# Optimization experiments

Measured on AMD Instinct MI355X. Metric: run time of the kernel, lower is better.

The kernel has to match this reference:

```python
import jax, jax.numpy as jnp
import numpy as np
import math

MAX_P = 150
D_MODEL = 128
N_HEADS = 4
D_HEAD = D_MODEL // N_HEADS
D_MLP = 512
D_MEM = 64
VOCAB = MAX_P + 2  # 152
EQ_TOKEN = MAX_P + 1  # 151
B = 65536


def setup_inputs() -> dict:
    key = jax.random.key(0)
    ks = jax.random.split(key, 20)
    s = 1.0 / math.sqrt(D_MODEL)
    inp = {
        "p_val": jax.random.randint(ks[0], (B,), 0, MAX_P),
        "a": jax.random.randint(ks[1], (B,), 0, MAX_P),
        "b": jax.random.randint(ks[2], (B,), 0, MAX_P),
        # embeddings
        "token_embed": jax.random.normal(ks[3], (VOCAB, D_MODEL), jnp.float32),
        "pos_embed": jax.random.normal(ks[4], (5, D_MODEL), jnp.float32),
        # TitansMemory
        "W_mem": jax.random.normal(ks[5], (D_MODEL, D_MEM), jnp.float32) * s,
        "b_mem": jnp.zeros((D_MEM,), jnp.float32),
        "W_sur": jax.random.normal(ks[6], (D_MEM, D_MODEL), jnp.float32) * (1.0 / math.sqrt(D_MEM)),
        "b_sur": jnp.zeros((D_MODEL,), jnp.float32),
        "W_m2r": jax.random.normal(ks[7], (D_MEM, D_MODEL), jnp.float32) * (1.0 / math.sqrt(D_MEM)),
        "b_m2r": jnp.zeros((D_MODEL,), jnp.float32),
        # attention
        "W_Q": jax.random.normal(ks[8], (N_HEADS, D_MODEL, D_HEAD), jnp.float32) * s,
        "W_K": jax.random.normal(ks[9], (N_HEADS, D_MODEL, D_HEAD), jnp.float32) * s,
        "W_V": jax.random.normal(ks[10], (N_HEADS, D_MODEL, D_HEAD), jnp.float32) * s,
        "W_O": jax.random.normal(ks[11], (N_HEADS, D_HEAD, D_MODEL), jnp.float32) * s,
        # MLP
        "W_mlp1": jax.random.normal(ks[12], (D_MODEL, D_MLP), jnp.float32) * s,
        "b_mlp1": jnp.zeros((D_MLP,), jnp.float32),
        "W_mlp2": jax.random.normal(ks[13], (D_MLP, D_MODEL), jnp.float32) * (1.0 / math.sqrt(D_MLP)),
        "b_mlp2": jnp.zeros((D_MODEL,), jnp.float32),
        # unembed
        "W_un": jax.random.normal(ks[14], (D_MODEL, MAX_P), jnp.float32) * s,
        "b_un": jnp.zeros((MAX_P,), jnp.float32),
    }
    return inp


def reference(p_val, a, b, token_embed, pos_embed, W_mem, b_mem, W_sur, b_sur,
              W_m2r, b_m2r, W_Q, W_K, W_V, W_O, W_mlp1, b_mlp1, W_mlp2, b_mlp2,
              W_un, b_un):
    eq = jnp.full_like(a, EQ_TOKEN)
    tokens = jnp.stack([p_val, a, b, eq], axis=1)            # [B, 4]
    x = token_embed[tokens] + pos_embed[:4][None, :, :]       # [B, 4, D]

    # Titans memory (test-time update) on the modulus token embedding
    x0 = x[:, 0, :]                                           # [B, D]
    z = jax.nn.silu(x0 @ W_mem + b_mem)                       # [B, d_mem]
    pred_x = z @ W_sur + b_sur                                # [B, D]
    update = jax.nn.silu((x0 - pred_x) @ W_mem)               # [B, d_mem]
    mem = (z + update) @ W_m2r + b_m2r                        # [B, D]
    x = x + mem[:, None, :]

    # attention
    q = jnp.einsum('bsd,hdk->bhsk', x, W_Q)
    k = jnp.einsum('bsd,hdk->bhsk', x, W_K)
    v = jnp.einsum('bsd,hdk->bhsk', x, W_V)
    scores = jnp.einsum('bhsk,bhtk->bhst', q, k) / math.sqrt(D_HEAD)
    pattern = jax.nn.softmax(scores, axis=-1)                 # [B, H, 4, 4]
    attn = jnp.einsum('bhst,bhtk->bhsk', pattern, v)
    attn = jnp.einsum('bhsk,hkm->bsm', attn, W_O)             # [B, 4, D]
    x = x + attn

    # MLP
    x = x + jax.nn.relu(x @ W_mlp1 + b_mlp1) @ W_mlp2 + b_mlp2

    # unembed the '=' position
    logits = x[:, 3, :] @ W_un + b_un                         # [B, max_p]
    return logits
```

## Files before the change

kernel.cpp:

```cpp
#include <hip/hip_runtime.h>

#define D      128
#define DM     64
#define DMLP   512
#define PMAX   150
#define VOC    152
#define EQT    151
#define NBATCH 65536

typedef __attribute__((ext_vector_type(8))) __bf16 bf16x8;
typedef __attribute__((ext_vector_type(4))) float  f32x4;

__device__ __forceinline__ float silu_f(float x){ return x / (1.0f + expf(-x)); }

__device__ __forceinline__ void gl_lds16(const void* g, void* l) {
    __builtin_amdgcn_global_load_lds(
        (const __attribute__((address_space(1))) void*)g,
        (__attribute__((address_space(3))) void*)l, 16, 0, 0);
}

#define OFF_MEMVEC 0
#define OFF_X3BASE 19200
#define OFF_KE     19328
#define OFF_KP     38784
#define OFF_SC     39296
#define OFF_O0     132896
#define OFF_O1     171296
#define OFF_O2     209696
#define OFF_O3     248096
#define OFF_M3B    248352
#define OFF_W1F    257952
#define OFF_W2F    290720
#define OFF_WUF    323488

__global__ void k_P1a(const float* __restrict__ tok, const float* __restrict__ pos,
                      const float* __restrict__ W_mem, const float* __restrict__ b_mem,
                      const float* __restrict__ W_sur, const float* __restrict__ b_sur,
                      const float* __restrict__ W_m2r, const float* __restrict__ b_m2r,
                      const float* __restrict__ W_K,
                      float* __restrict__ memvec, float* __restrict__ x3base,
                      float* __restrict__ KE, float* __restrict__ KP)
{
    int r = blockIdx.x, t = threadIdx.x;
    if (r < 150) {
        int p = r;
        __shared__ float sx0[D], sz[DM], sdiff[D], szu[DM], red4[4][DM], red2[2][D];
        if (t < D) sx0[t] = tok[p*D + t] + pos[t];
        __syncthreads();
        {
            int out = t & 63, seg = t >> 6, k0 = seg*32;
            float acc = 0.f;
            for (int k = 0; k < 32; k++) acc += sx0[k0+k] * W_mem[(k0+k)*DM + out];
            red4[seg][out] = acc;
        }
        __syncthreads();
        if (t < DM) sz[t] = silu_f(b_mem[t] + red4[0][t] + red4[1][t] + red4[2][t] + red4[3][t]);
        __syncthreads();
        {
            int out = t & 127, seg = t >> 7, j0 = seg*32;
            float acc = 0.f;
            for (int j = 0; j < 32; j++) acc += sz[j0+j] * W_sur[(j0+j)*D + out];
            red2[seg][out] = acc;
        }
        __syncthreads();
        if (t < D) sdiff[t] = sx0[t] - (b_sur[t] + red2[0][t] + red2[1][t]);
        __syncthreads();
        {
            int out = t & 63, seg = t >> 6, k0 = seg*32;
            float acc = 0.f;
            for (int k = 0; k < 32; k++) acc += sdiff[k0+k] * W_mem[(k0+k)*DM + out];
            red4[seg][out] = acc;
        }
        __syncthreads();
        if (t < DM) szu[t] = sz[t] + silu_f(red4[0][t] + red4[1][t] + red4[2][t] + red4[3][t]);
        __syncthreads();
        {
            int out = t & 127, seg = t >> 7, j0 = seg*32;
            float acc = 0.f;
            for (int j = 0; j < 32; j++) acc += szu[j0+j] * W_m2r[(j0+j)*D + out];
            red2[seg][out] = acc;
        }
        __syncthreads();
        if (t < D) memvec[p*D + t] = b_m2r[t] + red2[0][t] + red2[1][t];
    } else if (r == 150) {
        if (t < D) x3base[t] = tok[EQT*D + t] + pos[3*D + t];
    } else {
        int idx = r - 151;
        const float* src = (idx < 152) ? (tok + idx*D) : (pos + (idx-152)*D);
        float*       dst = (idx < 152) ? (KE + idx*D)  : (KP + (idx-152)*D);
        __shared__ float s[D], red2[2][D];
        if (t < D) s[t] = src[t];
        __syncthreads();
        {
            int out = t & 127, seg = t >> 7, h = out >> 5, kk = out & 31, d0 = seg*64;
            float acc = 0.f;
            for (int d = 0; d < 64; d++) acc += s[d0+d] * W_K[h*4096 + (d0+d)*32 + kk];
            red2[seg][out] = acc;
        }
        __syncthreads();
        if (t < D) dst[t] = red2[0][t] + red2[1][t];
    }
}

__global__ void k_P2x(const float* __restrict__ memvec, const float* __restrict__ x3base,
                      const float* __restrict__ W_Q, const float* __restrict__ W_V,
                      const float* __restrict__ W_O,
                      const float* __restrict__ KE, const float* __restrict__ KP,
                      const float* __restrict__ tok, const float* __restrict__ pos,
                      const float* __restrict__ W1, const float* __restrict__ W2,
                      const float* __restrict__ WU,
                      float* __restrict__ SC, __bf16* __restrict__ M3B,
                      __bf16* __restrict__ O0, __bf16* __restrict__ O1,
                      __bf16* __restrict__ O2, __bf16* __restrict__ O3,
                      __bf16* __restrict__ W1f, __bf16* __restrict__ W2f, __bf16* __restrict__ WUf)
{
    int r = blockIdx.x, t = threadIdx.x;
    if (r < 300) {
        int p = r >> 1, half = r & 1;
        __shared__ float sMem[D], sIn[D], sQ3[D], sMV[D], redM[2][D];
        if (t < D) { float m = memvec[p*D + t]; sMem[t] = m; sIn[t] = m + x3base[t]; }
        __syncthreads();
        if (t < D) {
            int h = t >> 5, k = t & 31;
            float acc = 0.f;
            for (int d = 0; d < D; d++) acc += sIn[d] * W_Q[h*4096 + d*32 + k];
            sQ3[t] = acc;
        } else {
            int c = t - D; int h = c >> 5, k = c & 31;
            float acc = 0.f;
            for (int d = 0; d < D; d++) acc += sMem[d] * W_V[h*4096 + d*32 + k];
            sMV[c] = acc;
        }
        __syncthreads();
        const float scale = 0.17677669529663687f;
        for (int ii = t; ii < 312; ii += 256) {
            int i = half*312 + ii;
            int v = i >> 2, h = i & 3;
            const float4* qh = (const float4*)(sQ3 + h*32);
            float4 s4 = {0.f, 0.f, 0.f, 0.f};
            if (v < 152) {
                const float4* ke = (const float4*)(KE + v*D + h*32);
                #pragma unroll
                for (int k = 0; k < 8; k++) {
                    float4 q = qh[k], e = ke[k];
                    s4.x += q.x*e.x; s4.y += q.y*e.y; s4.z += q.z*e.z; s4.w += q.w*e.w;
                }
            } else if (v == 152 || v == 153) {
                const float4* ke = (const float4*)(KE + ((v==152)? p : EQT)*D + h*32);
                const float4* kp = (const float4*)(KP + ((v==152)? 0 : 3)*D + h*32);
                #pragma unroll
                for (int k = 0; k < 8; k++) {
                    float4 q = qh[k], e = ke[k], pp = kp[k];
                    s4.x += q.x*(e.x+pp.x); s4.y += q.y*(e.y+pp.y);
                    s4.z += q.z*(e.z+pp.z); s4.w += q.w*(e.w+pp.w);
                }
            } else {
                const float4* kp = (const float4*)(KP + ((v==154)?1:2)*D + h*32);
                #pragma unroll
                for (int k = 0; k < 8; k++) {
                    float4 q = qh[k], pp = kp[k];
                    s4.x += q.x*pp.x; s4.y += q.y*pp.y; s4.z += q.z*pp.z; s4.w += q.w*pp.w;
                }
            }
            SC[p*624 + i] = (s4.x + s4.y + s4.z + s4.w) * scale;
        }
        if (half == 0) {
            {
                int out = t & 127, seg = t >> 7, c0 = seg*64;
                float acc = 0.f;
                for (int c = 0; c < 64; c++) acc += sMV[c0+c] * W_O[(c0+c)*D + out];
                redM[seg][out] = acc;
            }
            __syncthreads();
            if (t < D) M3B[p*D + t] = (__bf16)(sIn[t] + redM[0][t] + redM[1][t]);
        }
        return;
    }
    int rr = r - 300;
    if (rr < 451) {
        int idx = rr;
        int tt, v; __bf16* outp;
        if (idx < 150)      { tt = 0; v = idx;       outp = O0 + v*512; }
        else if (idx < 300) { tt = 1; v = idx - 150; outp = O1 + (idx-150)*512; }
        else if (idx < 450) { tt = 2; v = idx - 300; outp = O2 + (idx-300)*512; }
        else                { tt = 3; v = EQT;       outp = O3; }
        __shared__ float sTP[D], sv[D], red2[2][D];
        if (t < D) sTP[t] = tok[v*D + t] + pos[tt*D + t];
        __syncthreads();
        {
            int out = t & 127, seg = t >> 7, h = out >> 5, kk = out & 31, d0 = seg*64;
            float acc = 0.f;
            for (int d = 0; d < 64; d++) acc += sTP[d0+d] * W_V[h*4096 + (d0+d)*32 + kk];
            red2[seg][out] = acc;
        }
        __syncthreads();
        if (t < D) sv[t] = red2[0][t] + red2[1][t];
        __syncthreads();
        #pragma unroll
        for (int i = 0; i < 2; i++) {
            int c = t + i*256;
            int h = c >> 7, m = c & 127;
            float acc = 0.f;
            for (int k = 0; k < 32; k++) acc += sv[h*32 + k] * W_O[h*4096 + k*128 + m];
            outp[c] = (__bf16)acc;
        }
    } else if (rr < 483) {
        int f = (rr-451)*256 + t;
        int l = f & 63, kb = (f>>6) & 3, nb = f >> 8;
        int k0 = kb*32 + (l>>4)*8, n = nb*16 + (l&15);
        #pragma unroll
        for (int j = 0; j < 8; j++) W1f[f*8 + j] = (__bf16)W1[(k0+j)*DMLP + n];
    } else if (rr < 515) {
        int f = (rr-483)*256 + t;
        int l = f & 63, g = f >> 6;
        int nb = g & 7, kb = g >> 3;
        int k0 = kb*32 + (l>>4)*8, n = nb*16 + (l&15);
        #pragma unroll
        for (int j = 0; j < 8; j++) W2f[f*8 + j] = (__bf16)W2[(k0+j)*D + n];
    } else {
        int f = (rr-515)*256 + t;
        int l = f & 63, kb = (f>>6) & 3, nb = f >> 8;
        int k0 = kb*32 + (l>>4)*8, n = nb*16 + (l&15);
        #pragma unroll
        for (int j = 0; j < 8; j++) WUf[f*8 + j] = (__bf16)((n < 150) ? WU[(k0+j)*150 + n] : 0.f);
    }
}

__global__ __launch_bounds__(256, 4) void k_fused(
    const int* __restrict__ p_val, const int* __restrict__ a_tok, const int* __restrict__ b_tok,
    const float* __restrict__ SC, const __bf16* __restrict__ O0, const __bf16* __restrict__ O1,
    const __bf16* __restrict__ O2, const __bf16* __restrict__ O3g, const __bf16* __restrict__ M3B,
    const __bf16* __restrict__ W1f, const __bf16* __restrict__ W2f, const __bf16* __restrict__ WUf,
    const float* __restrict__ b1, const float* __restrict__ b2, const float* __restrict__ bun,
    float* __restrict__ out)
{
    __shared__ __align__(16) char smem[39936];
    char*  sX3 = smem + 8192;
    float* sB1 = (float*)(smem + 37888);

    int tid = threadIdx.x;
    int wv = tid >> 6, l = tid & 63, lr = l & 15, quad = l >> 4;
    int tbase = blockIdx.x * 64 + wv * 16;

    const char* gW1 = (const char*)W1f;
    const char* gW2 = (const char*)W2f;

    gl_lds16(gW1 + tid*16,       smem + tid*16);
    gl_lds16(gW1 + (tid+256)*16, smem + (tid+256)*16);
    gl_lds16(gW2 + tid*16,       smem + 24576 + tid*16);
    gl_lds16(gW2 + (tid+256)*16, smem + 24576 + (tid+256)*16);
    sB1[tid] = b1[tid]; sB1[tid+256] = b1[tid+256];

    {
        int s = tid >> 2, h = tid & 3;
        int gs = blockIdx.x * 64 + s;
        int p = p_val[gs], ta = a_tok[gs], tb = b_tok[gs];

        float wloc[4];
        {
            const float* SCp = SC + p*624;
            float sc0 = SCp[608 + h];
            float sc3 = SCp[612 + h];
            float sc1 = SCp[ta*4 + h] + SCp[616 + h];
            float sc2 = SCp[tb*4 + h] + SCp[620 + h];
            float mx = fmaxf(fmaxf(sc0, sc1), fmaxf(sc2, sc3));
            float e0 = expf(sc0-mx), e1 = expf(sc1-mx), e2 = expf(sc2-mx), e3 = expf(sc3-mx);
            float inv = 1.f / (e0 + e1 + e2 + e3);
            wloc[0] = e0*inv; wloc[1] = e1*inv; wloc[2] = e2*inv; wloc[3] = e3*inv;
        }
        float w[16];
        #pragma unroll
        for (int j = 0; j < 4; j++) w[h*4 + j] = wloc[j];
        #pragma unroll
        for (int m = 1; m < 4; m++) {
            int oh = h ^ m;
            #pragma unroll
            for (int j = 0; j < 4; j++) w[oh*4 + j] = __shfl_xor(wloc[j], m);
        }

        const bf16x8* m3v = (const bf16x8*)(M3B + p*128);
        const bf16x8* t0  = (const bf16x8*)(O0 + p*512);
        const bf16x8* t1  = (const bf16x8*)(O1 + ta*512);
        const bf16x8* t2  = (const bf16x8*)(O2 + tb*512);
        const bf16x8* t3  = (const bf16x8*)O3g;
        #pragma unroll
        for (int jj = 0; jj < 4; jj++) {
            int c8 = h*4 + jj;
            bf16x8 mv = m3v[c8];
            float v[8];
            #pragma unroll
            for (int e = 0; e < 8; e++) v[e] = (float)mv[e];
            #pragma unroll
            for (int hh = 0; hh < 4; hh++) {
                int o8 = hh*16 + c8;
                bf16x8 e0 = t0[o8], e1 = t1[o8], e2 = t2[o8], e3 = t3[o8];
                float w0 = w[hh*4+0], w1 = w[hh*4+1], w2 = w[hh*4+2], w3 = w[hh*4+3];
                #pragma unroll
                for (int e = 0; e < 8; e++)
                    v[e] += w0*(float)e0[e] + w1*(float)e1[e] + w2*(float)e2[e] + w3*(float)e3[e];
            }
            bf16x8 st;
            #pragma unroll
            for (int e = 0; e < 8; e++) st[e] = (__bf16)v[e];
            *(bf16x8*)(sX3 + s*256 + ((c8*16) ^ ((s&7)<<4))) = st;
        }
    }
    asm volatile("s_waitcnt lgkmcnt(0)" ::: "memory");
    __builtin_amdgcn_sched_barrier(0);

    bf16x8 a[4];
    {
        int arow = wv*16 + lr;
        #pragma unroll
        for (int kb = 0; kb < 4; kb++)
            a[kb] = *(const bf16x8*)(sX3 + arow*256 + ((kb*64 + quad*16) ^ ((lr&7)<<4)));
    }
    __syncthreads();

    char* sPanH = smem + 32768 + wv*1280;

    f32x4 acc2[8];
    #pragma unroll
    for (int i = 0; i < 8; i++) acc2[i] = (f32x4){0.f, 0.f, 0.f, 0.f};

    for (int cc = 0; cc < 16; cc++) {
        int pb = cc & 1;
        char* w1b = smem + pb*8192;
        char* w2b = smem + 16384 + (pb^1)*8192;
        if (cc < 15) {
            const char* g1 = gW1 + (cc+1)*8192;
            const char* g2 = gW2 + (cc+1)*8192;
            char* d1 = smem + (pb^1)*8192;
            char* d2 = smem + 16384 + pb*8192;
            gl_lds16(g1 + tid*16,       d1 + tid*16);
            gl_lds16(g1 + (tid+256)*16, d1 + (tid+256)*16);
            gl_lds16(g2 + tid*16,       d2 + tid*16);
            gl_lds16(g2 + (tid+256)*16, d2 + (tid+256)*16);
        }
        #pragma unroll
        for (int nbl = 0; nbl < 2; nbl++) {
            float bv = sB1[cc*32 + nbl*16 + lr];
            f32x4 acc = (f32x4){bv, bv, bv, bv};
            #pragma unroll
            for (int kb = 0; kb < 4; kb++) {
                bf16x8 w1 = *(const bf16x8*)(w1b + ((nbl*4 + kb)*64 + l)*16);
                acc = __builtin_amdgcn_mfma_f32_16x16x32_bf16(a[kb], w1, acc, 0, 0, 0);
            }
            #pragma unroll
            for (int r = 0; r < 4; r++)
                *(__bf16*)(sPanH + (((quad*4 + r)*40) + nbl*16 + lr)*2) = (__bf16)fmaxf(acc[r], 0.f);
        }
        asm volatile("s_waitcnt lgkmcnt(0)" ::: "memory");
        __builtin_amdgcn_sched_barrier(0);
        {
            bf16x8 h = *(const bf16x8*)(sPanH + (lr*40 + quad*8)*2);
            #pragma unroll
            for (int nb2 = 0; nb2 < 8; nb2++) {
                bf16x8 w2 = *(const bf16x8*)(w2b + (nb2*64 + l)*16);
                acc2[nb2] = __builtin_amdgcn_mfma_f32_16x16x32_bf16(h, w2, acc2[nb2], 0, 0, 0);
            }
        }
        __syncthreads();
    }

    float rb2[8], rbun[10];
    #pragma unroll
    for (int nb2 = 0; nb2 < 8; nb2++) rb2[nb2] = b2[nb2*16 + lr];
    #pragma unroll
    for (int nt = 0; nt < 10; nt++) {
        int n = nt*16 + lr;
        rbun[nt] = (n < 150) ? bun[n] : 0.f;
    }

    const char* gWU = (const char*)WUf;
    char* sWU = smem + 16384;
    gl_lds16(gWU + tid*16,       sWU + tid*16);
    gl_lds16(gWU + (tid+256)*16, sWU + (tid+256)*16);
    gl_lds16(gWU + (tid+512)*16, sWU + (tid+512)*16);
    gl_lds16(gWU + (tid+768)*16, sWU + (tid+768)*16);

    #pragma unroll
    for (int nb2 = 0; nb2 < 8; nb2++) {
        int kb = nb2 >> 1;
        bf16x8 bi;
        #pragma unroll
        for (int j = 0; j < 8; j++)
            bi[j] = (kb*32 + quad*8 + j == nb2*16 + lr) ? (__bf16)1.0f : (__bf16)0.0f;
        acc2[nb2] = __builtin_amdgcn_mfma_f32_16x16x32_bf16(a[kb], bi, acc2[nb2], 0, 0, 0);
    }

    #pragma unroll
    for (int nb2 = 0; nb2 < 8; nb2++) {
        int n = nb2*16 + lr;
        float bv = rb2[nb2];
        #pragma unroll
        for (int r = 0; r < 4; r++) {
            float v = acc2[nb2][r] + bv;
            int row = wv*16 + quad*4 + r;
            *(__bf16*)(smem + row*256 + ((n*2) ^ ((row&7)<<4))) = (__bf16)v;
        }
    }
    asm volatile("s_waitcnt lgkmcnt(0)" ::: "memory");
    __builtin_amdgcn_sched_barrier(0);
    bf16x8 au[4];
    {
        int arow = wv*16 + lr;
        #pragma unroll
        for (int kb = 0; kb < 4; kb++)
            au[kb] = *(const bf16x8*)(smem + arow*256 + ((kb*64 + quad*16) ^ ((lr&7)<<4)));
    }

    #pragma unroll
    for (int q = 0; q < 3; q++) {
        if (q == 1) {
            __syncthreads();
            const char* g = gWU + 16384;
            gl_lds16(g + tid*16,       sWU + tid*16);
            gl_lds16(g + (tid+256)*16, sWU + (tid+256)*16);
            gl_lds16(g + (tid+512)*16, sWU + (tid+512)*16);
            gl_lds16(g + (tid+768)*16, sWU + (tid+768)*16);
        } else if (q == 2) {
            __syncthreads();
            const char* g = gWU + 32768;
            gl_lds16(g + tid*16,       sWU + tid*16);
            gl_lds16(g + (tid+256)*16, sWU + (tid+256)*16);
        }
        __syncthreads();
        int ntn = (q < 2) ? 4 : 2;
        #pragma unroll
        for (int ntl = 0; ntl < ntn; ntl++) {
            int nt = q*4 + ntl;
            int n = nt*16 + lr;
            f32x4 acc = (f32x4){rbun[nt], rbun[nt], rbun[nt], rbun[nt]};
            #pragma unroll
            for (int kb = 0; kb < 4; kb++) {
                bf16x8 wu = *(const bf16x8*)(sWU + ((ntl*4 + kb)*64 + l)*16);
                acc = __builtin_amdgcn_mfma_f32_16x16x32_bf16(au[kb], wu, acc, 0, 0, 0);
            }
            if (n < 150) {
                #pragma unroll
                for (int r = 0; r < 4; r++) {
                    int rowg = tbase + quad*4 + r;
                    out[rowg*150 + n] = acc[r];
                }
            }
        }
    }
}

extern "C" void kernel_launch(void* const* d_in, const int* in_sizes, int n_in,
                              void* d_out, int out_size, void* d_ws, size_t ws_size,
                              hipStream_t stream) {
    const int*   p_val = (const int*)d_in[0];
    const int*   a_tok = (const int*)d_in[1];
    const int*   b_tok = (const int*)d_in[2];
    const float* tok   = (const float*)d_in[3];
    const float* pos   = (const float*)d_in[4];
    const float* W_mem = (const float*)d_in[5];
    const float* b_mem = (const float*)d_in[6];
    const float* W_sur = (const float*)d_in[7];
    const float* b_sur = (const float*)d_in[8];
    const float* W_m2r = (const float*)d_in[9];
    const float* b_m2r = (const float*)d_in[10];
    const float* W_Q   = (const float*)d_in[11];
    const float* W_K   = (const float*)d_in[12];
    const float* W_V   = (const float*)d_in[13];
    const float* W_O   = (const float*)d_in[14];
    const float* W1    = (const float*)d_in[15];
    const float* b1    = (const float*)d_in[16];
    const float* W2    = (const float*)d_in[17];
    const float* b2    = (const float*)d_in[18];
    const float* WU    = (const float*)d_in[19];
    const float* bun   = (const float*)d_in[20];
    float* out = (float*)d_out;

    float* ws = (float*)d_ws;
    float* memvec = ws + OFF_MEMVEC;
    float* x3base = ws + OFF_X3BASE;
    float* KE     = ws + OFF_KE;
    float* KP     = ws + OFF_KP;
    float* SC     = ws + OFF_SC;
    __bf16* O0    = (__bf16*)(ws + OFF_O0);
    __bf16* O1    = (__bf16*)(ws + OFF_O1);
    __bf16* O2    = (__bf16*)(ws + OFF_O2);
    __bf16* O3    = (__bf16*)(ws + OFF_O3);
    __bf16* M3B   = (__bf16*)(ws + OFF_M3B);
    __bf16* W1f   = (__bf16*)(ws + OFF_W1F);
    __bf16* W2f   = (__bf16*)(ws + OFF_W2F);
    __bf16* WUf   = (__bf16*)(ws + OFF_WUF);

    k_P1a<<<307, 256, 0, stream>>>(tok, pos, W_mem, b_mem, W_sur, b_sur, W_m2r, b_m2r,
                                   W_K, memvec, x3base, KE, KP);
    k_P2x<<<825, 256, 0, stream>>>(memvec, x3base, W_Q, W_V, W_O, KE, KP,
                                   tok, pos, W1, W2, WU,
                                   SC, M3B, O0, O1, O2, O3, W1f, W2f, WUf);
    k_fused<<<NBATCH/64, 256, 0, stream>>>(p_val, a_tok, b_tok, SC, O0, O1, O2, O3, M3B,
                                           W1f, W2f, WUf, b1, b2, bun, out);
}
```

Measured before the change: 172.3 us.

## Software-pipeline MLP chunks so layer-2 MFMAs overlap next chunk's layer-1

Restructures the MLP chunk loop into a prologue, steady state and epilogue. Each iteration computes layer-1 for chunk cc while the layer-2 MFMAs consume the hidden panel of chunk cc-1, read into registers first. The W2 prefetch schedule shifts by one chunk to match. This removes the intra-iteration wait between writing the hidden panel to LDS and reading it back, at the cost of more complex buffer indexing and extra register pressure from holding hprev.

```diff
diff --git a/kernel.cpp b/kernel.cpp
--- a/kernel.cpp
+++ b/kernel.cpp
@@ -247,8 +247,6 @@
 
     gl_lds16(gW1 + tid*16,       smem + tid*16);
     gl_lds16(gW1 + (tid+256)*16, smem + (tid+256)*16);
-    gl_lds16(gW2 + tid*16,       smem + 24576 + tid*16);
-    gl_lds16(gW2 + (tid+256)*16, smem + 24576 + (tid+256)*16);
     sB1[tid] = b1[tid]; sB1[tid+256] = b1[tid+256];
 
     {
@@ -323,42 +321,77 @@
     #pragma unroll
     for (int i = 0; i < 8; i++) acc2[i] = (f32x4){0.f, 0.f, 0.f, 0.f};
 
-    for (int cc = 0; cc < 16; cc++) {
-        int pb = cc & 1;
-        char* w1b = smem + pb*8192;
-        char* w2b = smem + 16384 + (pb^1)*8192;
+    {
+        const char* g1 = gW1 + 8192;
+        gl_lds16(g1 + tid*16,       smem + 8192 + tid*16);
+        gl_lds16(g1 + (tid+256)*16, smem + 8192 + (tid+256)*16);
+        gl_lds16(gW2 + tid*16,       smem + 16384 + tid*16);
+        gl_lds16(gW2 + (tid+256)*16, smem + 16384 + (tid+256)*16);
+        #pragma unroll
+        for (int nbl = 0; nbl < 2; nbl++) {
+            float bv = sB1[nbl*16 + lr];
+            f32x4 acc = (f32x4){bv, bv, bv, bv};
+            #pragma unroll
+            for (int kb = 0; kb < 4; kb++) {
+                bf16x8 w1 = *(const bf16x8*)(smem + ((nbl*4 + kb)*64 + l)*16);
+                acc = __builtin_amdgcn_mfma_f32_16x16x32_bf16(a[kb], w1, acc, 0, 0, 0);
+            }
+            #pragma unroll
+            for (int r = 0; r < 4; r++)
+                *(__bf16*)(sPanH + (((quad*4 + r)*40) + nbl*16 + lr)*2) = (__bf16)fmaxf(acc[r], 0.f);
+        }
+        __syncthreads();
+    }
+
+    for (int cc = 1; cc < 16; cc++) {
         if (cc < 15) {
             const char* g1 = gW1 + (cc+1)*8192;
-            const char* g2 = gW2 + (cc+1)*8192;
-            char* d1 = smem + (pb^1)*8192;
-            char* d2 = smem + 16384 + pb*8192;
+            char* d1 = smem + ((cc+1)&1)*8192;
             gl_lds16(g1 + tid*16,       d1 + tid*16);
             gl_lds16(g1 + (tid+256)*16, d1 + (tid+256)*16);
+        }
+        {
+            const char* g2 = gW2 + cc*8192;
+            char* d2 = smem + 16384 + (cc&1)*8192;
             gl_lds16(g2 + tid*16,       d2 + tid*16);
             gl_lds16(g2 + (tid+256)*16, d2 + (tid+256)*16);
         }
-        #pragma unroll
-        for (int nbl = 0; nbl < 2; nbl++) {
-            float bv = sB1[cc*32 + nbl*16 + lr];
-            f32x4 acc = (f32x4){bv, bv, bv, bv};
-            #pragma unroll
-            for (int kb = 0; kb < 4; kb++) {
-                bf16x8 w1 = *(const bf16x8*)(w1b + ((nbl*4 + kb)*64 + l)*16);
-                acc = __builtin_amdgcn_mfma_f32_16x16x32_bf16(a[kb], w1, acc, 0, 0, 0);
-            }
-            #pragma unroll
-            for (int r = 0; r < 4; r++)
-                *(__bf16*)(sPanH + (((quad*4 + r)*40) + nbl*16 + lr)*2) = (__bf16)fmaxf(acc[r], 0.f);
-        }
-        asm volatile("s_waitcnt lgkmcnt(0)" ::: "memory");
+        bf16x8 hprev = *(const bf16x8*)(sPanH + (lr*40 + quad*8)*2);
         __builtin_amdgcn_sched_barrier(0);
         {
-            bf16x8 h = *(const bf16x8*)(sPanH + (lr*40 + quad*8)*2);
+            char* w1b = smem + (cc&1)*8192;
+            #pragma unroll
+            for (int nbl = 0; nbl < 2; nbl++) {
+                float bv = sB1[cc*32 + nbl*16 + lr];
+                f32x4 acc = (f32x4){bv, bv, bv, bv};
+                #pragma unroll
+                for (int kb = 0; kb < 4; kb++) {
+                    bf16x8 w1 = *(const bf16x8*)(w1b + ((nbl*4 + kb)*64 + l)*16);
+                    acc = __builtin_amdgcn_mfma_f32_16x16x32_bf16(a[kb], w1, acc, 0, 0, 0);
+                }
+                #pragma unroll
+                for (int r = 0; r < 4; r++)
+                    *(__bf16*)(sPanH + (((quad*4 + r)*40) + nbl*16 + lr)*2) = (__bf16)fmaxf(acc[r], 0.f);
+            }
+        }
+        {
+            char* w2b = smem + 16384 + ((cc-1)&1)*8192;
             #pragma unroll
             for (int nb2 = 0; nb2 < 8; nb2++) {
                 bf16x8 w2 = *(const bf16x8*)(w2b + (nb2*64 + l)*16);
-                acc2[nb2] = __builtin_amdgcn_mfma_f32_16x16x32_bf16(h, w2, acc2[nb2], 0, 0, 0);
-            }
+                acc2[nb2] = __builtin_amdgcn_mfma_f32_16x16x32_bf16(hprev, w2, acc2[nb2], 0, 0, 0);
+            }
+        }
+        __syncthreads();
+    }
+
+    {
+        bf16x8 hprev = *(const bf16x8*)(sPanH + (lr*40 + quad*8)*2);
+        char* w2b = smem + 16384 + 8192;
+        #pragma unroll
+        for (int nb2 = 0; nb2 < 8; nb2++) {
+            bf16x8 w2 = *(const bf16x8*)(w2b + (nb2*64 + l)*16);
+            acc2[nb2] = __builtin_amdgcn_mfma_f32_16x16x32_bf16(hprev, w2, acc2[nb2], 0, 0, 0);
         }
         __syncthreads();
     }
```

Result: slower. 189.1 us (+9.7%).
